# Performance work log

Measured on AMD Instinct MI355X. Metric: run time of the kernel, lower is better.

## Reference

```python
import jax, jax.numpy as jnp
import numpy as np

NC, NB, NT = 512, 128, 256   # feats dims: [channels, batch, time]
H = 512                      # hidden_size
NCLS = 97                    # num_classes
NUM_STEPS = 32               # fixed decode length (= text_length.max())


def setup_inputs() -> dict:
    key = jax.random.key(0)
    ks = jax.random.split(key, 12)
    s = 1.0 / np.sqrt(H)
    inp = {
        "feats": jax.random.normal(ks[0], (NC, NB, NT), jnp.float32),
        "text_length": jnp.full((NB,), NUM_STEPS, jnp.int32),
        # AttentionCell params
        "Wi2h": jax.random.normal(ks[1], (H, NC), jnp.float32) * s,   # i2h, no bias
        "Wh2h": jax.random.normal(ks[2], (H, H), jnp.float32) * s,
        "bh2h": jax.random.normal(ks[3], (H,), jnp.float32) * s,
        "Wscore": jax.random.normal(ks[4], (1, H), jnp.float32) * s,  # score, no bias
        # GRUCell params (gate order: r, z, n as in PyTorch)
        "Wih": jax.random.normal(ks[5], (3 * H, NC), jnp.float32) * s,
        "Whh": jax.random.normal(ks[6], (3 * H, H), jnp.float32) * s,
        "bih": jax.random.normal(ks[7], (3 * H,), jnp.float32) * s,
        "bhh": jax.random.normal(ks[8], (3 * H,), jnp.float32) * s,
        # generator: Linear(hidden_size, num_classes - 1)
        "Wgen": jax.random.normal(ks[9], (NCLS - 1, H), jnp.float32) * s,
        "bgen": jax.random.normal(ks[10], (NCLS - 1,), jnp.float32) * s,
    }
    return inp


def reference(feats, text_length, Wi2h, Wh2h, bh2h, Wscore, Wih, Whh, bih, bhh, Wgen, bgen):
    # feats: [nC, nB, nT]
    nC, nB, nT = feats.shape
    # i2h(feats) is step-independent -> hoist out of the loop (same math)
    feats_proj = jnp.einsum('cbt,hc->bth', feats, Wi2h)  # [nB, nT, H]
    w_score = Wscore[0]                                   # [H]

    def step(h, _):
        # additive attention
        hp = h @ Wh2h.T + bh2h                                  # [nB, H]
        e = jnp.tanh(feats_proj + hp[:, None, :]) @ w_score     # [nB, nT]
        alpha = jax.nn.softmax(e, axis=1)                       # [nB, nT]
        context = jnp.einsum('cbt,bt->bc', feats, alpha)        # [nB, nC]
        # GRUCell(context, h), PyTorch semantics
        gi = context @ Wih.T + bih                              # [nB, 3H]
        gh = h @ Whh.T + bhh                                    # [nB, 3H]
        ir, iz, in_ = jnp.split(gi, 3, axis=1)
        hr, hz, hn = jnp.split(gh, 3, axis=1)
        r = jax.nn.sigmoid(ir + hr)
        z = jax.nn.sigmoid(iz + hz)
        n = jnp.tanh(in_ + r * hn)
        h_new = (1.0 - z) * n + z * h
        return h_new, h_new

    h0 = jnp.zeros((nB, feats_proj.shape[-1]), feats.dtype)
    _, hiddens = jax.lax.scan(step, h0, None, length=NUM_STEPS)  # [T, nB, H]
    # all lengths == NUM_STEPS -> gather is a per-batch flatten
    new_hiddens = hiddens.transpose(1, 0, 2).reshape(-1, hiddens.shape[-1])  # [nB*T, H]
    probs = new_hiddens @ Wgen.T + bgen                          # [nB*T, NCLS-1]
    return probs
```

## Files before the change

### kernel.cpp

```cpp
#include <hip/hip_runtime.h>
#include <math.h>

#define NBATCH 128
#define NTIME  256
#define NCH    512
#define NH     512
#define NSTEPS 32
#define NOUT   96
#define MTOT   32768

typedef __attribute__((ext_vector_type(8))) short short8v;
typedef __attribute__((ext_vector_type(4))) float f32x4;

__device__ __forceinline__ float fast_tanh(float x) {
    x = fminf(fmaxf(x, -30.f), 30.f);
    float u = __expf(2.f * x);
    return (u - 1.f) / (u + 1.f);
}
__device__ __forceinline__ float fast_sigmoid(float x) {
    x = fminf(fmaxf(x, -30.f), 30.f);
    return 1.f / (1.f + __expf(-x));
}
__device__ __forceinline__ float wave_reduce_sum(float s) {
    #pragma unroll
    for (int off = 32; off; off >>= 1) s += __shfl_xor(s, off, 64);
    return s;
}
__device__ __forceinline__ float wave_reduce_max(float s) {
    #pragma unroll
    for (int off = 32; off; off >>= 1) s = fmaxf(s, __shfl_xor(s, off, 64));
    return s;
}
__device__ __forceinline__ unsigned short f2bf(float f) {
    unsigned u = __builtin_bit_cast(unsigned, f);
    return (unsigned short)((u + 0x7FFFu + ((u >> 16) & 1u)) >> 16);
}

__global__ __launch_bounds__(256) void k_fp_gemm(const float* __restrict__ feats,
                                                 const float* __restrict__ Wi2h,
                                                 float* __restrict__ fp) {
    __shared__ float As[16][128];
    __shared__ float Bs[16][132];
    const int m0 = (blockIdx.x & 255) * 128;
    const int n0 = (blockIdx.x >> 8) * 128;
    const int tid = threadIdx.x;
    const int tx = tid & 15, ty = tid >> 4;
    float acc[8][8] = {};
    for (int k0 = 0; k0 < NCH; k0 += 16) {
        #pragma unroll
        for (int i = 0; i < 2; ++i) {
            int f4 = tid + i * 256;
            int kk = f4 >> 5, mm4 = (f4 & 31) << 2;
            *(float4*)(&As[kk][mm4]) =
                *(const float4*)(feats + (size_t)(k0 + kk) * MTOT + m0 + mm4);
        }
        #pragma unroll
        for (int i = 0; i < 2; ++i) {
            int f4 = tid + i * 256;
            int nn = f4 >> 2, kq = (f4 & 3) << 2;
            float4 v = *(const float4*)(Wi2h + (size_t)(n0 + nn) * NCH + k0 + kq);
            Bs[kq + 0][nn] = v.x; Bs[kq + 1][nn] = v.y;
            Bs[kq + 2][nn] = v.z; Bs[kq + 3][nn] = v.w;
        }
        __syncthreads();
        #pragma unroll
        for (int kk = 0; kk < 16; ++kk) {
            float a[8], b[8];
            *(float4*)(a)     = *(const float4*)(&As[kk][ty * 8]);
            *(float4*)(a + 4) = *(const float4*)(&As[kk][ty * 8 + 4]);
            *(float4*)(b)     = *(const float4*)(&Bs[kk][tx * 8]);
            *(float4*)(b + 4) = *(const float4*)(&Bs[kk][tx * 8 + 4]);
            #pragma unroll
            for (int i = 0; i < 8; ++i)
                #pragma unroll
                for (int j = 0; j < 8; ++j) acc[i][j] += a[i] * b[j];
        }
        __syncthreads();
    }
    #pragma unroll
    for (int i = 0; i < 8; ++i) {
        float* dst = fp + (size_t)(m0 + ty * 8 + i) * NH + n0 + tx * 8;
        *(float4*)(dst)     = *(float4*)(&acc[i][0]);
        *(float4*)(dst + 4) = *(float4*)(&acc[i][4]);
    }
}

__global__ __launch_bounds__(256) void k_w2bf(const float* __restrict__ W,
                                              unsigned short* __restrict__ Wb) {
    #pragma unroll
    for (int r = 0; r < 4; ++r) {
        int idx = (blockIdx.x * 256 + threadIdx.x) + r * 16384;
        float4 v = *(const float4*)(W + (size_t)idx * 4);
        ushort4 o;
        o.x = f2bf(v.x); o.y = f2bf(v.y); o.z = f2bf(v.z); o.w = f2bf(v.w);
        *(ushort4*)(Wb + (size_t)idx * 4) = o;
    }
}

__global__ __launch_bounds__(256) void k_feats2bf(const float* __restrict__ feats,
                                                  unsigned short* __restrict__ Fb) {
    __shared__ float tl[64][65];
    const int m0 = (blockIdx.x & 511) * 64;
    const int k0 = (blockIdx.x >> 9) * 64;
    const int tid = threadIdx.x;
    #pragma unroll
    for (int p = 0; p < 4; ++p) {
        int fid = tid + p * 256;
        int row = fid >> 4, c4 = fid & 15;
        float4 v = *(const float4*)(feats + (size_t)(k0 + row) * MTOT + m0 + c4 * 4);
        tl[row][c4 * 4 + 0] = v.x; tl[row][c4 * 4 + 1] = v.y;
        tl[row][c4 * 4 + 2] = v.z; tl[row][c4 * 4 + 3] = v.w;
    }
    __syncthreads();
    #pragma unroll
    for (int p = 0; p < 4; ++p) {
        int cid = tid + p * 256;
        int mm = cid >> 4, ch = cid & 15;
        ushort4 o;
        o.x = f2bf(tl[ch * 4 + 0][mm]);
        o.y = f2bf(tl[ch * 4 + 1][mm]);
        o.z = f2bf(tl[ch * 4 + 2][mm]);
        o.w = f2bf(tl[ch * 4 + 3][mm]);
        *(ushort4*)(Fb + (size_t)(m0 + mm) * 512 + k0 + ch * 4) = o;
    }
}

__global__ __launch_bounds__(256) void k_fp_mfma(const unsigned short* __restrict__ Wb,
                                                 const unsigned short* __restrict__ Fb,
                                                 float* __restrict__ fp) {
    __shared__ unsigned short As[128 * 64];
    __shared__ unsigned short Bs[256 * 64];
    const int m0 = (blockIdx.x & 127) * 256;
    const int h0 = (blockIdx.x >> 7) * 128;
    const int tid = threadIdx.x;
    const int lane = tid & 63, wid = tid >> 6;
    const int wh = wid & 1, wm = wid >> 1;
    f32x4 acc[4][8];
    #pragma unroll
    for (int i = 0; i < 4; ++i)
        #pragma unroll
        for (int j = 0; j < 8; ++j) acc[i][j] = (f32x4)0.f;

    for (int k0 = 0; k0 < 512; k0 += 64) {
        #pragma unroll
        for (int i = 0; i < 4; ++i) {
            int cid = tid + i * 256;
            int row = cid >> 3, ch = cid & 7;
            uint4 v = *(const uint4*)(Wb + (size_t)(h0 + row) * 512 + k0 + ch * 8);
            *(uint4*)(As + row * 64 + ((ch ^ (row & 7)) << 3)) = v;
        }
        #pragma unroll
        for (int i = 0; i < 8; ++i) {
            int cid = tid + i * 256;
            int row = cid >> 3, ch = cid & 7;
            uint4 v = *(const uint4*)(Fb + (size_t)(m0 + row) * 512 + k0 + ch * 8);
            *(uint4*)(Bs + row * 64 + ((ch ^ (row & 7)) << 3)) = v;
        }
        __syncthreads();
        #pragma unroll
        for (int ks = 0; ks < 2; ++ks) {
            short8v a[4], b[8];
            #pragma unroll
            for (int hf = 0; hf < 4; ++hf) {
                int row = wh * 64 + hf * 16 + (lane & 15);
                int ch = ks * 4 + (lane >> 4);
                a[hf] = *(const short8v*)(As + row * 64 + ((ch ^ (row & 7)) << 3));
            }
            #pragma unroll
            for (int mf = 0; mf < 8; ++mf) {
                int row = wm * 128 + mf * 16 + (lane & 15);
                int ch = ks * 4 + (lane >> 4);
                b[mf] = *(const short8v*)(Bs + row * 64 + ((ch ^ (row & 7)) << 3));
            }
            #pragma unroll
            for (int hf = 0; hf < 4; ++hf)
                #pragma unroll
                for (int mf = 0; mf < 8; ++mf)
                    acc[hf][mf] = __builtin_amdgcn_mfma_f32_16x16x32_bf16(
                        a[hf], b[mf], acc[hf][mf], 0, 0, 0);
        }
        __syncthreads();
    }
    #pragma unroll
    for (int hf = 0; hf < 4; ++hf) {
        int h = h0 + wh * 64 + hf * 16 + (lane >> 4) * 4;
        #pragma unroll
        for (int mf = 0; mf < 8; ++mf) {
            int m = m0 + wm * 128 + mf * 16 + (lane & 15);
            *(f32x4*)(fp + (size_t)m * 512 + h) = acc[hf][mf];
        }
    }
}

__global__ __launch_bounds__(256) void k_wt(const float* __restrict__ W,
                                            float* __restrict__ WT) {
    __shared__ float tl[32][33];
    const int bi = blockIdx.x & 15, bj = blockIdx.x >> 4;
    const int tx = threadIdx.x & 31, ty8 = threadIdx.x >> 5;
    #pragma unroll
    for (int i = 0; i < 4; ++i) {
        int r = ty8 * 4 + i;
        tl[r][tx] = W[(size_t)(bj * 32 + r) * NH + bi * 32 + tx];
    }
    __syncthreads();
    #pragma unroll
    for (int i = 0; i < 4; ++i) {
        int c = ty8 * 4 + i;
        WT[(size_t)(bi * 32 + c) * NH + bj * 32 + tx] = tl[tx][c];
    }
}

__global__ __launch_bounds__(1024) void k_hp0(const float* __restrict__ bh2h,
                                              float* __restrict__ hp) {
    int i = blockIdx.x * 1024 + threadIdx.x;
    hp[i] = bh2h[i & 511];
}

__global__ __launch_bounds__(512) void k_e(const float* __restrict__ fp,
                                           const float* __restrict__ hp,
                                           const float* __restrict__ wscore,
                                           float* __restrict__ e) {
    const int b = blockIdx.x >> 2;
    const int t0 = (blockIdx.x & 3) * 64;
    const int tid = threadIdx.x;
    const int lane = tid & 63, w = tid >> 6;
    float4 h0 = *(const float4*)(hp + (size_t)b * NH + lane * 8);
    float4 h1 = *(const float4*)(hp + (size_t)b * NH + lane * 8 + 4);
    float4 w0 = *(const float4*)(wscore + lane * 8);
    float4 w1 = *(const float4*)(wscore + lane * 8 + 4);
    #pragma unroll 2
    for (int it = 0; it < 8; ++it) {
        int t = t0 + w * 8 + it;
        const float4* p = (const float4*)(fp + (size_t)(b * NTIME + t) * NH + lane * 8);
        float4 v0 = p[0], v1 = p[1];
        float s = fast_tanh(v0.x + h0.x) * w0.x + fast_tanh(v0.y + h0.y) * w0.y +
                  fast_tanh(v0.z + h0.z) * w0.z + fast_tanh(v0.w + h0.w) * w0.w +
                  fast_tanh(v1.x + h1.x) * w1.x + fast_tanh(v1.y + h1.y) * w1.y +
                  fast_tanh(v1.z + h1.z) * w1.z + fast_tanh(v1.w + h1.w) * w1.w;
        s = wave_reduce_sum(s);
        if (lane == 0) e[b * NTIME + t] = s;
    }
}

__global__ __launch_bounds__(512) void k_ctx2(const float* __restrict__ e,
                                              const float* __restrict__ feats,
                                              float* __restrict__ ctx) {
    __shared__ float als[256];
    __shared__ float red[8];
    const int b = blockIdx.x >> 2;
    const int c0 = (blockIdx.x & 3) * 128;
    const int tid = threadIdx.x;
    const int lane = tid & 63, w = tid >> 6;
    float v = (tid < 256) ? e[b * NTIME + tid] : -3.4e38f;
    float m = wave_reduce_max(v);
    if (lane == 0) red[w] = m;
    __syncthreads();
    m = red[0];
    #pragma unroll
    for (int i = 1; i < 8; ++i) m = fmaxf(m, red[i]);
    float ex = (tid < 256) ? __expf(v - m) : 0.f;
    float s = wave_reduce_sum(ex);
    __syncthreads();
    if (lane == 0) red[w] = s;
    __syncthreads();
    s = 0.f;
    #pragma unroll
    for (int i = 0; i < 8; ++i) s += red[i];
    if (tid < 256) als[tid] = ex / s;
    __syncthreads();

    float4 al = *(const float4*)&als[lane * 4];
    #pragma unroll 4
    for (int cc = 0; cc < 16; ++cc) {
        int c = c0 + w * 16 + cc;
        float4 f = *(const float4*)(feats + (size_t)(c * NBATCH + b) * NTIME + lane * 4);
        float sc = f.x * al.x + f.y * al.y + f.z * al.z + f.w * al.w;
        sc = wave_reduce_sum(sc);
        if (lane == 0) ctx[(size_t)b * NCH + c] = sc;
    }
}

__global__ __launch_bounds__(1024) void k_gates(const float* __restrict__ ctx,
                                                const float* __restrict__ h,
                                                const float* __restrict__ Wih,
                                                const float* __restrict__ Whh,
                                                float* __restrict__ g2) {
    __shared__ float S[16384 + 8192];
    float* A_ldsT = S;
    float* scr    = S + 16384;
    const int blk = blockIdx.x;
    const int g   = blk >> 5;
    const int j0  = (blk & 31) * 16;
    const float* A = (g < 3) ? ctx : h;
    const float* W = (g < 3) ? Wih : Whh;
    const int tid = threadIdx.x;
    const int m2  = tid & 63;
    const int q   = __builtin_amdgcn_readfirstlane(tid >> 6);
    const int nq  = q & 3, kq = q >> 2;
    const float* Wr0 = W + (size_t)((g % 3) * 512 + j0 + nq * 4 + 0) * NH;
    const float* Wr1 = W + (size_t)((g % 3) * 512 + j0 + nq * 4 + 1) * NH;
    const float* Wr2 = W + (size_t)((g % 3) * 512 + j0 + nq * 4 + 2) * NH;
    const float* Wr3 = W + (size_t)((g % 3) * 512 + j0 + nq * 4 + 3) * NH;
    float acc[2][4] = {};
    for (int kt = 0; kt < 4; ++kt) {
        {
            int m = tid & 127, kc = tid >> 7;
            #pragma unroll
            for (int q4 = 0; q4 < 4; ++q4) {
                int kk = kc * 16 + q4 * 4;
                float4 vv = *(const float4*)(A + (size_t)m * NH + kt * 128 + kk);
                A_ldsT[(kk + 0) * 128 + m] = vv.x;
                A_ldsT[(kk + 1) * 128 + m] = vv.y;
                A_ldsT[(kk + 2) * 128 + m] = vv.z;
                A_ldsT[(kk + 3) * 128 + m] = vv.w;
            }
        }
        __syncthreads();
        const int kbase = kt * 128;
        #pragma unroll 8
        for (int kk = kq * 32; kk < kq * 32 + 32; ++kk) {
            float a0 = A_ldsT[kk * 128 + m2];
            float a1 = A_ldsT[kk * 128 + m2 + 64];
            float w0 = Wr0[kbase + kk], w1 = Wr1[kbase + kk];
            float w2 = Wr2[kbase + kk], w3 = Wr3[kbase + kk];
            acc[0][0] += a0 * w0; acc[0][1] += a0 * w1;
            acc[0][2] += a0 * w2; acc[0][3] += a0 * w3;
            acc[1][0] += a1 * w0; acc[1][1] += a1 * w1;
            acc[1][2] += a1 * w2; acc[1][3] += a1 * w3;
        }
        __syncthreads();
    }
    #pragma unroll
    for (int hi = 0; hi < 2; ++hi)
        #pragma unroll
        for (int r = 0; r < 4; ++r)
            scr[(kq * 16 + nq * 4 + r) * 128 + m2 + 64 * hi] = acc[hi][r];
    __syncthreads();
    #pragma unroll
    for (int rep = 0; rep < 2; ++rep) {
        int oid = tid + rep * 1024;
        int m = oid & 127, nl = oid >> 7;
        float vv = scr[(0 * 16 + nl) * 128 + m] + scr[(1 * 16 + nl) * 128 + m] +
                   scr[(2 * 16 + nl) * 128 + m] + scr[(3 * 16 + nl) * 128 + m];
        g2[(size_t)(g * 512 + j0 + nl) * NBATCH + m] = vv;
    }
}

__global__ __launch_bounds__(1024) void k_comb_hp(const float* __restrict__ g2,
                                                  const float* __restrict__ hprev,
                                                  float* __restrict__ hidn,
                                                  const float* __restrict__ bih,
                                                  const float* __restrict__ bhh,
                                                  const float* __restrict__ WT,
                                                  const float* __restrict__ bh2h,
                                                  float* __restrict__ hp) {
    __shared__ float h_s[4 * 512];
    __shared__ float scr2[16 * 4 * 16 * 4];
    const int blk = blockIdx.x;
    const int b0 = (blk >> 3) * 4;
    const int jbase = (blk & 7) * 64;
    const int tid = threadIdx.x;
    #pragma unroll
    for (int rep = 0; rep < 2; ++rep) {
        int idx = tid + rep * 1024;
        int bi = idx & 3, kk = idx >> 2;
        int b = b0 + bi;
        float ir = g2[(size_t)(0 * 512 + kk) * NBATCH + b] + bih[kk];
        float iz = g2[(size_t)(1 * 512 + kk) * NBATCH + b] + bih[512 + kk];
        float in_ = g2[(size_t)(2 * 512 + kk) * NBATCH + b] + bih[1024 + kk];
        float hr = g2[(size_t)(3 * 512 + kk) * NBATCH + b] + bhh[kk];
        float hz = g2[(size_t)(4 * 512 + kk) * NBATCH + b] + bhh[512 + kk];
        float hn = g2[(size_t)(5 * 512 + kk) * NBATCH + b] + bhh[1024 + kk];
        float r = fast_sigmoid(ir + hr);
        float z = fast_sigmoid(iz + hz);
        float ng = fast_tanh(in_ + r * hn);
        float hv = hprev[(size_t)b * NH + kk];
        float hnew = (1.f - z) * ng + z * hv;
        h_s[bi * 512 + kk] = hnew;
        if ((blk & 7) == 0) hidn[(size_t)b * NH + kk] = hnew;
    }
    __syncthreads();
    {
        const int jq = tid & 15, bi = (tid >> 4) & 3, kq = tid >> 6;
        const int j = jbase + jq * 4;
        float4 acc = make_float4(0.f, 0.f, 0.f, 0.f);
        #pragma unroll 8
        for (int kk = 0; kk < 32; ++kk) {
            int k = kq * 32 + kk;
            float4 wv = *(const float4*)(WT + (size_t)k * NH + j);
            float hv = h_s[bi * 512 + k];
            acc.x += hv * wv.x; acc.y += hv * wv.y;
            acc.z += hv * wv.z; acc.w += hv * wv.w;
        }
        *(float4*)&scr2[((kq * 4 + bi) * 16 + jq) * 4] = acc;
    }
    __syncthreads();
    if (tid < 64) {
        const int bi = tid >> 4, jq = tid & 15;
        float4 sum = make_float4(0.f, 0.f, 0.f, 0.f);
        #pragma unroll
        for (int kq = 0; kq < 16; ++kq) {
            float4 p = *(const float4*)&scr2[((kq * 4 + bi) * 16 + jq) * 4];
            sum.x += p.x; sum.y += p.y; sum.z += p.z; sum.w += p.w;
        }
        int j = jbase + jq * 4;
        float4 bb = *(const float4*)(bh2h + j);
        sum.x += bb.x; sum.y += bb.y; sum.z += bb.z; sum.w += bb.w;
        *(float4*)(hp + (size_t)(b0 + bi) * NH + j) = sum;
    }
}

__global__ __launch_bounds__(256) void k_gen(const float* __restrict__ hid,
                                             const float* __restrict__ Wgen,
                                             const float* __restrict__ bgen,
                                             float* __restrict__ out) {
    __shared__ float As[32][36];
    __shared__ float Bs[32][97];
    const int m0 = blockIdx.x * 32;
    const int tid = threadIdx.x;
    const int tx = tid & 31, ty = tid >> 5;
    float acc[4][3] = {};
    for (int k0 = 0; k0 < 512; k0 += 32) {
        {
            int mm = tid >> 3, kq = (tid & 7) << 2;
            int m = m0 + mm, s = m & 31, b = m >> 5;
            float4 v = *(const float4*)(hid + (size_t)(s + 1) * 65536 + b * 512 + k0 + kq);
            *(float4*)(&As[mm][kq]) = v;
        }
        #pragma unroll
        for (int i = 0; i < 3; ++i) {
            int f4 = tid + i * 256;
            int nn = f4 >> 3, kq = (f4 & 7) << 2;
            float4 v = *(const float4*)(Wgen + (size_t)nn * 512 + k0 + kq);
            Bs[kq + 0][nn] = v.x; Bs[kq + 1][nn] = v.y;
            Bs[kq + 2][nn] = v.z; Bs[kq + 3][nn] = v.w;
        }
        __syncthreads();
        #pragma unroll
        for (int kk = 0; kk < 32; ++kk) {
            float bv[3];
            #pragma unroll
            for (int j = 0; j < 3; ++j) bv[j] = Bs[kk][tx * 3 + j];
            #pragma unroll
            for (int i = 0; i < 4; ++i) {
                float a = As[ty * 4 + i][kk];
                #pragma unroll
                for (int j = 0; j < 3; ++j) acc[i][j] += a * bv[j];
            }
        }
        __syncthreads();
    }
    #pragma unroll
    for (int i = 0; i < 4; ++i)
        #pragma unroll
        for (int j = 0; j < 3; ++j)
            out[(size_t)(m0 + ty * 4 + i) * NOUT + tx * 3 + j] = acc[i][j] + bgen[tx * 3 + j];
}

extern "C" void kernel_launch(void* const* d_in, const int* in_sizes, int n_in,
                              void* d_out, int out_size, void* d_ws, size_t ws_size,
                              hipStream_t stream) {
    const float* feats  = (const float*)d_in[0];
    const float* Wi2h   = (const float*)d_in[2];
    const float* Wh2h   = (const float*)d_in[3];
    const float* bh2h   = (const float*)d_in[4];
    const float* Wscore = (const float*)d_in[5];
    const float* Wih    = (const float*)d_in[6];
    const float* Whh    = (const float*)d_in[7];
    const float* bih    = (const float*)d_in[8];
    const float* bhh    = (const float*)d_in[9];
    const float* Wgen   = (const float*)d_in[10];
    const float* bgen   = (const float*)d_in[11];
    float* out = (float*)d_out;

    float* ws  = (float*)d_ws;
    float* fp    = ws;
    float* hid   = fp + 16777216;
    float* WT    = hid + 2162688;
    float* hpctx = WT + 262144;
    unsigned short* W_b = (unsigned short*)(hpctx + 65536);
    unsigned short* Fb  = (unsigned short*)(hpctx + 65536 + 131072);
    const size_t need_big = (size_t)(16777216 + 2162688 + 262144 + 65536 + 131072 + 8388608) * 4;
    const bool big = ws_size >= need_big;

    float* e  = out;
    float* g2 = out;

    hipMemsetAsync(hid, 0, 65536 * sizeof(float), stream);
    k_wt<<<256, 256, 0, stream>>>(Wh2h, WT);
    if (big) {
        k_w2bf<<<64, 256, 0, stream>>>(Wi2h, W_b);
        k_feats2bf<<<4096, 256, 0, stream>>>(feats, Fb);
        k_fp_mfma<<<512, 256, 0, stream>>>(W_b, Fb, fp);
    } else {
        k_fp_gemm<<<1024, 256, 0, stream>>>(feats, Wi2h, fp);
    }
    k_hp0<<<64, 1024, 0, stream>>>(bh2h, hpctx);

    for (int s = 0; s < NSTEPS; ++s) {
        const float* h = hid + (size_t)s * 65536;
        float* hn      = hid + (size_t)(s + 1) * 65536;
        k_e<<<512, 512, 0, stream>>>(fp, hpctx, Wscore, e);
        k_ctx2<<<512, 512, 0, stream>>>(e, feats, hpctx);
        k_gates<<<192, 1024, 0, stream>>>(hpctx, h, Wih, Whh, g2);
        k_comb_hp<<<256, 1024, 0, stream>>>(g2, h, hn, bih, bhh, WT, bh2h, hpctx);
    }
    k_gen<<<128, 256, 0, stream>>>(hid, Wgen, bgen, out);
}
```

Measured before the change: 1.852 ms.

## Store projected features and feats in bf16 to halve per-step memory traffic

The projected feature tensor is now written as bf16 from the MFMA GEMM, staged through LDS so the stores coalesce. A bf16 copy of feats is also made once, in its original layout, for the context kernel. Both per-step kernels (score and context) then read half as many bytes from the 32-step loop's large tensors, which were bandwidth-bound. The fp32 fallback GEMM and the workspace-size check are removed, which adds precision loss in the attention scores and context and assumes the workspace is large enough.

```diff
diff --git a/kernel.cpp b/kernel.cpp
--- a/kernel.cpp
+++ b/kernel.cpp
@@ -35,54 +35,11 @@
     unsigned u = __builtin_bit_cast(unsigned, f);
     return (unsigned short)((u + 0x7FFFu + ((u >> 16) & 1u)) >> 16);
 }
-
-__global__ __launch_bounds__(256) void k_fp_gemm(const float* __restrict__ feats,
-                                                 const float* __restrict__ Wi2h,
-                                                 float* __restrict__ fp) {
-    __shared__ float As[16][128];
-    __shared__ float Bs[16][132];
-    const int m0 = (blockIdx.x & 255) * 128;
-    const int n0 = (blockIdx.x >> 8) * 128;
-    const int tid = threadIdx.x;
-    const int tx = tid & 15, ty = tid >> 4;
-    float acc[8][8] = {};
-    for (int k0 = 0; k0 < NCH; k0 += 16) {
-        #pragma unroll
-        for (int i = 0; i < 2; ++i) {
-            int f4 = tid + i * 256;
-            int kk = f4 >> 5, mm4 = (f4 & 31) << 2;
-            *(float4*)(&As[kk][mm4]) =
-                *(const float4*)(feats + (size_t)(k0 + kk) * MTOT + m0 + mm4);
-        }
-        #pragma unroll
-        for (int i = 0; i < 2; ++i) {
-            int f4 = tid + i * 256;
-            int nn = f4 >> 2, kq = (f4 & 3) << 2;
-            float4 v = *(const float4*)(Wi2h + (size_t)(n0 + nn) * NCH + k0 + kq);
-            Bs[kq + 0][nn] = v.x; Bs[kq + 1][nn] = v.y;
-            Bs[kq + 2][nn] = v.z; Bs[kq + 3][nn] = v.w;
-        }
-        __syncthreads();
-        #pragma unroll
-        for (int kk = 0; kk < 16; ++kk) {
-            float a[8], b[8];
-            *(float4*)(a)     = *(const float4*)(&As[kk][ty * 8]);
-            *(float4*)(a + 4) = *(const float4*)(&As[kk][ty * 8 + 4]);
-            *(float4*)(b)     = *(const float4*)(&Bs[kk][tx * 8]);
-            *(float4*)(b + 4) = *(const float4*)(&Bs[kk][tx * 8 + 4]);
-            #pragma unroll
-            for (int i = 0; i < 8; ++i)
-                #pragma unroll
-                for (int j = 0; j < 8; ++j) acc[i][j] += a[i] * b[j];
-        }
-        __syncthreads();
-    }
-    #pragma unroll
-    for (int i = 0; i < 8; ++i) {
-        float* dst = fp + (size_t)(m0 + ty * 8 + i) * NH + n0 + tx * 8;
-        *(float4*)(dst)     = *(float4*)(&acc[i][0]);
-        *(float4*)(dst + 4) = *(float4*)(&acc[i][4]);
-    }
+__device__ __forceinline__ float bflo(unsigned u) {
+    return __builtin_bit_cast(float, u << 16);
+}
+__device__ __forceinline__ float bfhi(unsigned u) {
+    return __builtin_bit_cast(float, u & 0xFFFF0000u);
 }
 
 __global__ __launch_bounds__(256) void k_w2bf(const float* __restrict__ W,
@@ -125,11 +82,22 @@
     }
 }
 
+__global__ __launch_bounds__(1024) void k_fcopy(const float* __restrict__ f,
+                                                unsigned short* __restrict__ o) {
+    int gid = blockIdx.x * 1024 + threadIdx.x;
+    float4 v = *(const float4*)(f + (size_t)gid * 4);
+    ushort4 s;
+    s.x = f2bf(v.x); s.y = f2bf(v.y); s.z = f2bf(v.z); s.w = f2bf(v.w);
+    *(ushort4*)(o + (size_t)gid * 4) = s;
+}
+
 __global__ __launch_bounds__(256) void k_fp_mfma(const unsigned short* __restrict__ Wb,
                                                  const unsigned short* __restrict__ Fb,
-                                                 float* __restrict__ fp) {
-    __shared__ unsigned short As[128 * 64];
-    __shared__ unsigned short Bs[256 * 64];
+                                                 unsigned short* __restrict__ fp_bf) {
+    __shared__ char SB[49152];
+    unsigned short* As = (unsigned short*)SB;
+    unsigned short* Bs = (unsigned short*)(SB + 16384);
+    float* tl = (float*)SB;
     const int m0 = (blockIdx.x & 127) * 256;
     const int h0 = (blockIdx.x >> 7) * 128;
     const int tid = threadIdx.x;
@@ -183,12 +151,30 @@
     }
     #pragma unroll
     for (int hf = 0; hf < 4; ++hf) {
-        int h = h0 + wh * 64 + hf * 16 + (lane >> 4) * 4;
         #pragma unroll
         for (int mf = 0; mf < 8; ++mf) {
-            int m = m0 + wm * 128 + mf * 16 + (lane & 15);
-            *(f32x4*)(fp + (size_t)m * 512 + h) = acc[hf][mf];
-        }
+            int ml = wm * 128 + mf * 16 + (lane & 15);
+            int col = wh * 16 + (lane >> 4) * 4;
+            tl[ml * 33 + col + 0] = acc[hf][mf][0];
+            tl[ml * 33 + col + 1] = acc[hf][mf][1];
+            tl[ml * 33 + col + 2] = acc[hf][mf][2];
+            tl[ml * 33 + col + 3] = acc[hf][mf][3];
+        }
+        __syncthreads();
+        #pragma unroll
+        for (int mi = 0; mi < 8; ++mi) {
+            int ml = (tid >> 3) + mi * 32;
+            int hl4 = (tid & 7) * 4;
+            float v0 = tl[ml * 33 + hl4 + 0];
+            float v1 = tl[ml * 33 + hl4 + 1];
+            float v2 = tl[ml * 33 + hl4 + 2];
+            float v3 = tl[ml * 33 + hl4 + 3];
+            int hg = h0 + ((hl4 < 16) ? (hf * 16 + hl4) : (64 + hf * 16 + hl4 - 16));
+            ushort4 o;
+            o.x = f2bf(v0); o.y = f2bf(v1); o.z = f2bf(v2); o.w = f2bf(v3);
+            *(ushort4*)(fp_bf + (size_t)(m0 + ml) * 512 + hg) = o;
+        }
+        __syncthreads();
     }
 }
 
@@ -216,7 +202,7 @@
     hp[i] = bh2h[i & 511];
 }
 
-__global__ __launch_bounds__(512) void k_e(const float* __restrict__ fp,
+__global__ __launch_bounds__(512) void k_e(const unsigned short* __restrict__ fp_bf,
                                            const float* __restrict__ hp,
                                            const float* __restrict__ wscore,
                                            float* __restrict__ e) {
@@ -231,19 +217,18 @@
     #pragma unroll 2
     for (int it = 0; it < 8; ++it) {
         int t = t0 + w * 8 + it;
-        const float4* p = (const float4*)(fp + (size_t)(b * NTIME + t) * NH + lane * 8);
-        float4 v0 = p[0], v1 = p[1];
-        float s = fast_tanh(v0.x + h0.x) * w0.x + fast_tanh(v0.y + h0.y) * w0.y +
-                  fast_tanh(v0.z + h0.z) * w0.z + fast_tanh(v0.w + h0.w) * w0.w +
-                  fast_tanh(v1.x + h1.x) * w1.x + fast_tanh(v1.y + h1.y) * w1.y +
-                  fast_tanh(v1.z + h1.z) * w1.z + fast_tanh(v1.w + h1.w) * w1.w;
+        uint4 v = *(const uint4*)(fp_bf + (size_t)(b * NTIME + t) * NH + lane * 8);
+        float s = fast_tanh(bflo(v.x) + h0.x) * w0.x + fast_tanh(bfhi(v.x) + h0.y) * w0.y +
+                  fast_tanh(bflo(v.y) + h0.z) * w0.z + fast_tanh(bfhi(v.y) + h0.w) * w0.w +
+                  fast_tanh(bflo(v.z) + h1.x) * w1.x + fast_tanh(bfhi(v.z) + h1.y) * w1.y +
+                  fast_tanh(bflo(v.w) + h1.z) * w1.z + fast_tanh(bfhi(v.w) + h1.w) * w1.w;
         s = wave_reduce_sum(s);
         if (lane == 0) e[b * NTIME + t] = s;
     }
 }
 
 __global__ __launch_bounds__(512) void k_ctx2(const float* __restrict__ e,
-                                              const float* __restrict__ feats,
+                                              const unsigned short* __restrict__ featsb,
                                               float* __restrict__ ctx) {
     __shared__ float als[256];
     __shared__ float red[8];
@@ -273,8 +258,9 @@
     #pragma unroll 4
     for (int cc = 0; cc < 16; ++cc) {
         int c = c0 + w * 16 + cc;
-        float4 f = *(const float4*)(feats + (size_t)(c * NBATCH + b) * NTIME + lane * 4);
-        float sc = f.x * al.x + f.y * al.y + f.z * al.z + f.w * al.w;
+        uint2 fv = *(const uint2*)(featsb + (size_t)(c * NBATCH + b) * NTIME + lane * 4);
+        float sc = bflo(fv.x) * al.x + bfhi(fv.x) * al.y +
+                   bflo(fv.y) * al.z + bfhi(fv.y) * al.w;
         sc = wave_reduce_sum(sc);
         if (lane == 0) ctx[(size_t)b * NCH + c] = sc;
     }
@@ -474,34 +460,30 @@
     float* out = (float*)d_out;
 
     float* ws  = (float*)d_ws;
-    float* fp    = ws;
-    float* hid   = fp + 16777216;
+    unsigned short* fp_bf = (unsigned short*)ws;
+    float* hid   = ws + 8388608;
     float* WT    = hid + 2162688;
     float* hpctx = WT + 262144;
-    unsigned short* W_b = (unsigned short*)(hpctx + 65536);
-    unsigned short* Fb  = (unsigned short*)(hpctx + 65536 + 131072);
-    const size_t need_big = (size_t)(16777216 + 2162688 + 262144 + 65536 + 131072 + 8388608) * 4;
-    const bool big = ws_size >= need_big;
+    unsigned short* Wb     = (unsigned short*)(hpctx + 65536);
+    unsigned short* Fb     = (unsigned short*)(hpctx + 65536 + 131072);
+    unsigned short* featsb = Fb;
 
     float* e  = out;
     float* g2 = out;
 
     hipMemsetAsync(hid, 0, 65536 * sizeof(float), stream);
     k_wt<<<256, 256, 0, stream>>>(Wh2h, WT);
-    if (big) {
-        k_w2bf<<<64, 256, 0, stream>>>(Wi2h, W_b);
-        k_feats2bf<<<4096, 256, 0, stream>>>(feats, Fb);
-        k_fp_mfma<<<512, 256, 0, stream>>>(W_b, Fb, fp);
-    } else {
-        k_fp_gemm<<<1024, 256, 0, stream>>>(feats, Wi2h, fp);
-    }
+    k_w2bf<<<64, 256, 0, stream>>>(Wi2h, Wb);
+    k_feats2bf<<<4096, 256, 0, stream>>>(feats, Fb);
+    k_fp_mfma<<<512, 256, 0, stream>>>(Wb, Fb, fp_bf);
+    k_fcopy<<<4096, 1024, 0, stream>>>(feats, featsb);
     k_hp0<<<64, 1024, 0, stream>>>(bh2h, hpctx);
 
     for (int s = 0; s < NSTEPS; ++s) {
         const float* h = hid + (size_t)s * 65536;
         float* hn      = hid + (size_t)(s + 1) * 65536;
-        k_e<<<512, 512, 0, stream>>>(fp, hpctx, Wscore, e);
-        k_ctx2<<<512, 512, 0, stream>>>(e, feats, hpctx);
+        k_e<<<512, 512, 0, stream>>>(fp_bf, hpctx, Wscore, e);
+        k_ctx2<<<512, 512, 0, stream>>>(e, featsb, hpctx);
         k_gates<<<192, 1024, 0, stream>>>(hpctx, h, Wih, Whh, g2);
         k_comb_hp<<<256, 1024, 0, stream>>>(g2, h, hn, bih, bhh, WT, bh2h, hpctx);
     }
```

Measured after the change: 1.852 ms. No clear change (+0.0%).
